# Kernel tuning notes

Measured on AMD Instinct MI355X. Metric: run time of the kernel, lower is better.

## Reference

```python
import jax, jax.numpy as jnp
import numpy as np

STRIDE = 2

def setup_inputs() -> dict:
    key = jax.random.key(0)
    k1, k2 = jax.random.split(key)
    x = jax.random.normal(k1, (32, 128, 112, 112), dtype=jnp.float32)
    # matches nn.init.normal_(std=0.1)
    weight = jax.random.normal(k2, (256, 128, 3, 3), dtype=jnp.float32) * 0.1
    return {"x": x, "weight": weight}

def reference(x, weight):
    # Equivalent to the tile-loop: valid cross-correlation, no bias, stride=STRIDE.
    # x: (B, Cin, H, W); weight: (Cout, Cin, k, k) -> (B, Cout, w, w)
    return jax.lax.conv_general_dilated(
        x, weight,
        window_strides=(STRIDE, STRIDE),
        padding="VALID",
        dimension_numbers=("NCHW", "OIHW", "NCHW"),
    )
```

## Files before the change

### kernel.cpp

```cpp
#include <hip/hip_runtime.h>


#define BATCH 32
#define CIN   128
#define H     112
#define W     112
#define COUT  256
#define OH    55
#define OW    55
#define NPIX  (OH*OW)
#define NTOT  (BATCH*NPIX)

#define BN    192
#define NBLK  ((NTOT + BN - 1) / BN)

typedef __bf16 bf16x8 __attribute__((ext_vector_type(8)));
typedef float  f32x4  __attribute__((ext_vector_type(4)));

__device__ __forceinline__ unsigned short f2bf(float f) {
    unsigned u = __float_as_uint(f);
    u += 0x7FFFu + ((u >> 16) & 1u);
    return (unsigned short)(u >> 16);
}

__device__ __forceinline__ void gld_lds16(const void* g, void* l) {
    __builtin_amdgcn_global_load_lds((__attribute__((address_space(1))) void*)g,
                                     (__attribute__((address_space(3))) void*)l,
                                     16, 0, 0);
}

#define XP 136
#define WBLK ((9*COUT*CIN + 255)/256)
__global__ __launch_bounds__(256) void relayout_k(const float* __restrict__ x,
                                                  const float* __restrict__ w,
                                                  unsigned short* __restrict__ xs,
                                                  unsigned short* __restrict__ wt) {
    if (blockIdx.x >= BATCH * H) {
        int o = (blockIdx.x - BATCH * H) * 256 + threadIdx.x;
        if (o < 9 * COUT * CIN) {
            int cin  = o & (CIN - 1);
            int r    = o >> 7;
            int cout = r & (COUT - 1);
            int tap  = r >> 8;
            wt[o] = f2bf(w[((size_t)cout * CIN + cin) * 9 + tap]);
        }
        return;
    }
    __shared__ __align__(16) unsigned short tile[W * XP];
    const int bh = blockIdx.x;
    const int b  = bh / H;
    const int h  = bh - b * H;
    const float* xr = x + (size_t)b * CIN * (H * W) + (size_t)h * W;
    const int t = threadIdx.x;
#pragma unroll
    for (int i = 0; i < 7; ++i) {
        int e  = t + i * 256;
        int cp = e / 28;
        int w4 = e - cp * 28;
        int c  = cp * 2;
        float4 v0 = *(const float4*)(xr + (size_t)c * (H * W) + w4 * 4);
        float4 v1 = *(const float4*)(xr + (size_t)(c + 1) * (H * W) + w4 * 4);
        int c8 = c >> 3;
        int cl = c & 7;
        float a0[4] = {v0.x, v0.y, v0.z, v0.w};
        float a1[4] = {v1.x, v1.y, v1.z, v1.w};
#pragma unroll
        for (int j = 0; j < 4; ++j) {
            int ww  = w4 * 4 + j;
            int idx = ww * XP + ((c8 + 2 * ww) & 15) * 8 + cl;
            *(ushort2*)(tile + idx) = (ushort2){f2bf(a0[j]), f2bf(a1[j])};
        }
    }
    __syncthreads();
    uint4* dst = (uint4*)(xs + (size_t)bh * (W * CIN));
#pragma unroll
    for (int i = 0; i < 7; ++i) {
        int e  = t + i * 256;
        int ww = e >> 4;
        int c8 = e & 15;
        dst[e] = *(const uint4*)(tile + ww * XP + ((c8 + 2 * ww) & 15) * 8);
    }
}

__global__ __launch_bounds__(512, 2) void conv_mfma_k(const unsigned short* __restrict__ xs,
                                                      const unsigned short* __restrict__ wt,
                                                      float* __restrict__ out) {
    __shared__ __align__(16) unsigned short L[2][(COUT + BN) * 64];

    const int tid  = threadIdx.x;
    const int wave = tid >> 6;
    const int lane = tid & 63;
    const int wm   = wave >> 2;
    const int wn   = wave & 3;
    const int lrow = lane & 15;
    const int kg   = lane >> 4;
    const int n0   = blockIdx.x * BN;

    const int rA  = tid >> 3;
    const int sx8 = ((tid & 7) ^ (rA & 7)) * 8;
    int xbr[3];
#pragma unroll
    for (int c = 0; c < 3; ++c) {
        int nn = n0 + c * 64 + rA;
        if (nn >= NTOT) nn = NTOT - 1;
        int b  = nn / NPIX;
        int rp = nn - b * NPIX;
        int oh = rp / OW;
        int ow = rp - oh * OW;
        xbr[c] = ((b * H + 2 * oh) * W + 2 * ow) * CIN;
    }

    auto stage = [&](int kt, int buf) {
        const int tap  = kt >> 1;
        const int cin0 = (kt & 1) * 64;
        const int r    = (tap >= 6) ? 2 : (tap >= 3) ? 1 : 0;
        const int s    = tap - 3 * r;
        const unsigned short* wsrc = wt + tap * (COUT * CIN) + rA * CIN + cin0 + sx8;
        const unsigned short* xsrc = xs + (r * W + s) * CIN + cin0 + sx8;
        unsigned short* lb = &L[buf][0];
#pragma unroll
        for (int c = 0; c < 4; ++c)
            gld_lds16(wsrc + c * 64 * CIN, lb + c * 4096 + wave * 512);
#pragma unroll
        for (int c = 0; c < 3; ++c)
            gld_lds16(xsrc + xbr[c], lb + 16384 + c * 4096 + wave * 512);
    };

    const int aoff = (wm * 128 + lrow) * 64;
    const int boff = COUT * 64 + (wn * 48 + lrow) * 64;
    const int sxk0 = ((0 * 4 + kg) ^ (lrow & 7)) * 8;
    const int sxk1 = ((1 * 4 + kg) ^ (lrow & 7)) * 8;

    f32x4 acc[8][3];
#pragma unroll
    for (int mi = 0; mi < 8; ++mi)
#pragma unroll
        for (int ni = 0; ni < 3; ++ni)
            acc[mi][ni] = (f32x4){0.f, 0.f, 0.f, 0.f};

    stage(0, 0);
    stage(1, 1);

#pragma unroll 2
    for (int kt = 0; kt < 18; ++kt) {
        const int buf = kt & 1;
        if (kt == 17) asm volatile("s_waitcnt vmcnt(0)" ::: "memory");
        else          asm volatile("s_waitcnt vmcnt(7)" ::: "memory");
        asm volatile("s_barrier" ::: "memory");

        const unsigned short* Lb = &L[buf][0];
        bf16x8 a0[8], b0[3], a1[8], b1[3];
#pragma unroll
        for (int mi = 0; mi < 8; ++mi)
            a0[mi] = *(const bf16x8*)(Lb + aoff + mi * 1024 + sxk0);
#pragma unroll
        for (int ni = 0; ni < 3; ++ni)
            b0[ni] = *(const bf16x8*)(Lb + boff + ni * 1024 + sxk0);
        asm volatile("s_barrier" ::: "memory");
#pragma unroll
        for (int mi = 0; mi < 8; ++mi)
            a1[mi] = *(const bf16x8*)(Lb + aoff + mi * 1024 + sxk1);
#pragma unroll
        for (int ni = 0; ni < 3; ++ni)
            b1[ni] = *(const bf16x8*)(Lb + boff + ni * 1024 + sxk1);
        __builtin_amdgcn_s_setprio(1);
#pragma unroll
        for (int mi = 0; mi < 8; ++mi)
#pragma unroll
            for (int ni = 0; ni < 3; ++ni)
                acc[mi][ni] = __builtin_amdgcn_mfma_f32_16x16x32_bf16(a0[mi], b0[ni], acc[mi][ni], 0, 0, 0);
        __builtin_amdgcn_s_setprio(0);
        asm volatile("s_barrier" ::: "memory");
        if (kt + 2 < 18) stage(kt + 2, buf);
        __builtin_amdgcn_s_setprio(1);
#pragma unroll
        for (int mi = 0; mi < 8; ++mi)
#pragma unroll
            for (int ni = 0; ni < 3; ++ni)
                acc[mi][ni] = __builtin_amdgcn_mfma_f32_16x16x32_bf16(a1[mi], b1[ni], acc[mi][ni], 0, 0, 0);
        __builtin_amdgcn_s_setprio(0);
    }

    long obase[3];
    int  okn[3];
#pragma unroll
    for (int ni = 0; ni < 3; ++ni) {
        int nn = n0 + wn * 48 + ni * 16 + lrow;
        okn[ni] = (nn < NTOT);
        if (!okn[ni]) nn = 0;
        int b   = nn / NPIX;
        int pix = nn - b * NPIX;
        obase[ni] = (long)b * (COUT * NPIX) + pix;
    }
    const int mrow = kg * 4;
#pragma unroll
    for (int mi = 0; mi < 8; ++mi) {
#pragma unroll
        for (int rr = 0; rr < 4; ++rr) {
            int  m  = wm * 128 + mi * 16 + mrow + rr;
            long mo = (long)m * NPIX;
#pragma unroll
            for (int ni = 0; ni < 3; ++ni)
                if (okn[ni]) out[obase[ni] + mo] = acc[mi][ni][rr];
        }
    }
}

__global__ __launch_bounds__(256) void direct_k(const float* __restrict__ x,
                                                const float* __restrict__ w,
                                                float* __restrict__ out) {
    const int pix = blockIdx.x * 256 + threadIdx.x;
    if (pix >= NPIX) return;
    const int b = blockIdx.z, cout0 = blockIdx.y * 8;
    const int oh = pix / OW, ow = pix - oh * OW;
    float acc[8];
#pragma unroll
    for (int i = 0; i < 8; ++i) acc[i] = 0.f;
    const float* xbp = x + ((size_t)b * CIN) * (H * W) + (size_t)(oh * 2) * W + ow * 2;
    const float* wb  = w + (size_t)cout0 * (CIN * 9);
    for (int cin = 0; cin < CIN; ++cin) {
        const float* xp = xbp + (size_t)cin * (H * W);
        float xv[9];
#pragma unroll
        for (int r = 0; r < 3; ++r) {
            xv[r * 3 + 0] = xp[r * W + 0];
            xv[r * 3 + 1] = xp[r * W + 1];
            xv[r * 3 + 2] = xp[r * W + 2];
        }
#pragma unroll
        for (int c = 0; c < 8; ++c) {
            const float* wp = wb + (size_t)c * (CIN * 9) + cin * 9;
#pragma unroll
            for (int k = 0; k < 9; ++k) acc[c] = fmaf(wp[k], xv[k], acc[c]);
        }
    }
    const size_t ob = ((size_t)b * COUT + cout0) * NPIX + pix;
#pragma unroll
    for (int c = 0; c < 8; ++c) out[ob + (size_t)c * NPIX] = acc[c];
}

extern "C" void kernel_launch(void* const* d_in, const int* in_sizes, int n_in,
                              void* d_out, int out_size, void* d_ws, size_t ws_size,
                              hipStream_t stream) {
    const float* x = (const float*)d_in[0];
    const float* w = (const float*)d_in[1];
    float* out = (float*)d_out;

    const size_t xs_elems = (size_t)BATCH * H * W * CIN;
    const size_t wt_elems = (size_t)9 * COUT * CIN;
    const size_t need = (xs_elems + wt_elems) * 2;

    if (ws_size >= need) {
        unsigned short* xs = (unsigned short*)d_ws;
        unsigned short* wt = xs + xs_elems;
        relayout_k<<<dim3(BATCH * H + WBLK), dim3(256), 0, stream>>>(x, w, xs, wt);
        conv_mfma_k<<<dim3(NBLK), dim3(512), 0, stream>>>(xs, wt, out);
    } else {
        dim3 grid((NPIX + 255) / 256, COUT / 8, BATCH);
        direct_k<<<grid, dim3(256), 0, stream>>>(x, w, out);
    }
}
```

Measured before the change: 382.3 us.

## Interleave LDS fragment loads with MFMA halves and swizzle blocks across XCDs

Splits each k-step's A fragments into low and high halves, so MFMA work on one half overlaps the LDS reads for the next half. This also cuts live A registers from 16 vectors to 8. Block indices are remapped so that contiguous pixel tiles land on the same XCD, which should improve L2 reuse of the overlapping input windows. The finer interleave relies on compiler scheduling and could add LDS wait stalls between the MFMA groups.

```diff
diff --git a/kernel.cpp b/kernel.cpp
--- a/kernel.cpp
+++ b/kernel.cpp
@@ -94,7 +94,12 @@
     const int wn   = wave & 3;
     const int lrow = lane & 15;
     const int kg   = lane >> 4;
-    const int n0   = blockIdx.x * BN;
+
+    const int xcd = blockIdx.x & 7;
+    const int lin = blockIdx.x >> 3;
+    const int q = NBLK >> 3, r = NBLK & 7;
+    const int bswz = (xcd < r ? xcd * (q + 1) : r * (q + 1) + (xcd - r) * q) + lin;
+    const int n0 = bswz * BN;
 
     const int rA  = tid >> 3;
     const int sx8 = ((tid & 7) ^ (rA & 7)) * 8;
@@ -113,10 +118,10 @@
     auto stage = [&](int kt, int buf) {
         const int tap  = kt >> 1;
         const int cin0 = (kt & 1) * 64;
-        const int r    = (tap >= 6) ? 2 : (tap >= 3) ? 1 : 0;
-        const int s    = tap - 3 * r;
+        const int r2   = (tap >= 6) ? 2 : (tap >= 3) ? 1 : 0;
+        const int s    = tap - 3 * r2;
         const unsigned short* wsrc = wt + tap * (COUT * CIN) + rA * CIN + cin0 + sx8;
-        const unsigned short* xsrc = xs + (r * W + s) * CIN + cin0 + sx8;
+        const unsigned short* xsrc = xs + (r2 * W + s) * CIN + cin0 + sx8;
         unsigned short* lb = &L[buf][0];
 #pragma unroll
         for (int c = 0; c < 4; ++c)
@@ -149,35 +154,55 @@
         asm volatile("s_barrier" ::: "memory");
 
         const unsigned short* Lb = &L[buf][0];
-        bf16x8 a0[8], b0[3], a1[8], b1[3];
-#pragma unroll
-        for (int mi = 0; mi < 8; ++mi)
-            a0[mi] = *(const bf16x8*)(Lb + aoff + mi * 1024 + sxk0);
+        bf16x8 aL[4], aH[4], b0[3], b1[3];
+#pragma unroll
+        for (int mi = 0; mi < 4; ++mi)
+            aL[mi] = *(const bf16x8*)(Lb + aoff + mi * 1024 + sxk0);
 #pragma unroll
         for (int ni = 0; ni < 3; ++ni)
             b0[ni] = *(const bf16x8*)(Lb + boff + ni * 1024 + sxk0);
         asm volatile("s_barrier" ::: "memory");
-#pragma unroll
-        for (int mi = 0; mi < 8; ++mi)
-            a1[mi] = *(const bf16x8*)(Lb + aoff + mi * 1024 + sxk1);
+        __builtin_amdgcn_s_setprio(1);
+#pragma unroll
+        for (int mi = 0; mi < 4; ++mi)
+#pragma unroll
+            for (int ni = 0; ni < 3; ++ni)
+                acc[mi][ni] = __builtin_amdgcn_mfma_f32_16x16x32_bf16(aL[mi], b0[ni], acc[mi][ni], 0, 0, 0);
+        __builtin_amdgcn_s_setprio(0);
+#pragma unroll
+        for (int mi = 0; mi < 4; ++mi)
+            aH[mi] = *(const bf16x8*)(Lb + aoff + (mi + 4) * 1024 + sxk0);
+        __builtin_amdgcn_s_setprio(1);
+#pragma unroll
+        for (int mi = 0; mi < 4; ++mi)
+#pragma unroll
+            for (int ni = 0; ni < 3; ++ni)
+                acc[mi + 4][ni] = __builtin_amdgcn_mfma_f32_16x16x32_bf16(aH[mi], b0[ni], acc[mi + 4][ni], 0, 0, 0);
+        __builtin_amdgcn_s_setprio(0);
+#pragma unroll
+        for (int mi = 0; mi < 4; ++mi)
+            aL[mi] = *(const bf16x8*)(Lb + aoff + mi * 1024 + sxk1);
 #pragma unroll
         for (int ni = 0; ni < 3; ++ni)
             b1[ni] = *(const bf16x8*)(Lb + boff + ni * 1024 + sxk1);
         __builtin_amdgcn_s_setprio(1);
 #pragma unroll
-        for (int mi = 0; mi < 8; ++mi)
-#pragma unroll
-            for (int ni = 0; ni < 3; ++ni)
-                acc[mi][ni] = __builtin_amdgcn_mfma_f32_16x16x32_bf16(a0[mi], b0[ni], acc[mi][ni], 0, 0, 0);
-        __builtin_amdgcn_s_setprio(0);
+        for (int mi = 0; mi < 4; ++mi)
+#pragma unroll
+            for (int ni = 0; ni < 3; ++ni)
+                acc[mi][ni] = __builtin_amdgcn_mfma_f32_16x16x32_bf16(aL[mi], b1[ni], acc[mi][ni], 0, 0, 0);
+        __builtin_amdgcn_s_setprio(0);
+#pragma unroll
+        for (int mi = 0; mi < 4; ++mi)
+            aH[mi] = *(const bf16x8*)(Lb + aoff + (mi + 4) * 1024 + sxk1);
         asm volatile("s_barrier" ::: "memory");
         if (kt + 2 < 18) stage(kt + 2, buf);
         __builtin_amdgcn_s_setprio(1);
 #pragma unroll
-        for (int mi = 0; mi < 8; ++mi)
-#pragma unroll
-            for (int ni = 0; ni < 3; ++ni)
-                acc[mi][ni] = __builtin_amdgcn_mfma_f32_16x16x32_bf16(a1[mi], b1[ni], acc[mi][ni], 0, 0, 0);
+        for (int mi = 0; mi < 4; ++mi)
+#pragma unroll
+            for (int ni = 0; ni < 3; ++ni)
+                acc[mi + 4][ni] = __builtin_amdgcn_mfma_f32_16x16x32_bf16(aH[mi], b1[ni], acc[mi + 4][ni], 0, 0, 0);
         __builtin_amdgcn_s_setprio(0);
     }
 
@@ -197,7 +222,7 @@
     for (int mi = 0; mi < 8; ++mi) {
 #pragma unroll
         for (int rr = 0; rr < 4; ++rr) {
-            int  m  = wm * 128 + mi * 16 + mrow + rr;
+            int  m  = mi * 16 + mrow + rr + wm * 128;
             long mo = (long)m * NPIX;
 #pragma unroll
             for (int ni = 0; ni < 3; ++ni)
```

Result: no change. 381.8 us (-0.1%).

## Split output-channel tile into two 128-row blocks with XCD-aware block swizzle

Applied to the files above, without the earlier changes.

Each block of the implicit-GEMM conv now covers 128 of the 256 output channels with 4 waves (256 threads) instead of 8 waves, which doubles the grid. A chiplet-aware index remap places the two channel halves of the same pixel tile on the same XCD so they can share the input tile through L2. The inner loop now loads both k-halves from LDS before a single barrier, removing the mid-iteration barrier, and then issues all MFMAs together. The cost is twice as many input-tile loads per output, since each pixel tile is fetched by two blocks, and a larger per-wave MFMA footprint of 4x6.

```diff
diff --git a/kernel.cpp b/kernel.cpp
--- a/kernel.cpp
+++ b/kernel.cpp
@@ -11,8 +11,10 @@
 #define NPIX  (OH*OW)
 #define NTOT  (BATCH*NPIX)
 
+#define BM    128
 #define BN    192
-#define NBLK  ((NTOT + BN - 1) / BN)
+#define NB_N  ((NTOT + BN - 1) / BN)
+#define NBLK  (2 * NB_N)
 
 typedef __bf16 bf16x8 __attribute__((ext_vector_type(8)));
 typedef float  f32x4  __attribute__((ext_vector_type(4)));
@@ -82,26 +84,32 @@
     }
 }
 
-__global__ __launch_bounds__(512, 2) void conv_mfma_k(const unsigned short* __restrict__ xs,
+__global__ __launch_bounds__(256, 2) void conv_mfma_k(const unsigned short* __restrict__ xs,
                                                       const unsigned short* __restrict__ wt,
                                                       float* __restrict__ out) {
-    __shared__ __align__(16) unsigned short L[2][(COUT + BN) * 64];
+    __shared__ __align__(16) unsigned short L[2][(BM + BN) * 64];
 
     const int tid  = threadIdx.x;
     const int wave = tid >> 6;
     const int lane = tid & 63;
-    const int wm   = wave >> 2;
-    const int wn   = wave & 3;
+    const int wm   = wave >> 1;
+    const int wn   = wave & 1;
     const int lrow = lane & 15;
     const int kg   = lane >> 4;
-    const int n0   = blockIdx.x * BN;
+
+    const int xcd = blockIdx.x & 7;
+    const int lin = blockIdx.x >> 3;
+    const int q = NBLK >> 3, r = NBLK & 7;
+    const int bswz = (xcd < r ? xcd * (q + 1) : r * (q + 1) + (xcd - r) * q) + lin;
+    const int m0 = (bswz & 1) * BM;
+    const int n0 = (bswz >> 1) * BN;
 
     const int rA  = tid >> 3;
     const int sx8 = ((tid & 7) ^ (rA & 7)) * 8;
-    int xbr[3];
-#pragma unroll
-    for (int c = 0; c < 3; ++c) {
-        int nn = n0 + c * 64 + rA;
+    int xbr[6];
+#pragma unroll
+    for (int c = 0; c < 6; ++c) {
+        int nn = n0 + c * 32 + rA;
         if (nn >= NTOT) nn = NTOT - 1;
         int b  = nn / NPIX;
         int rp = nn - b * NPIX;
@@ -113,29 +121,29 @@
     auto stage = [&](int kt, int buf) {
         const int tap  = kt >> 1;
         const int cin0 = (kt & 1) * 64;
-        const int r    = (tap >= 6) ? 2 : (tap >= 3) ? 1 : 0;
-        const int s    = tap - 3 * r;
-        const unsigned short* wsrc = wt + tap * (COUT * CIN) + rA * CIN + cin0 + sx8;
-        const unsigned short* xsrc = xs + (r * W + s) * CIN + cin0 + sx8;
+        const int r2   = (tap >= 6) ? 2 : (tap >= 3) ? 1 : 0;
+        const int s    = tap - 3 * r2;
+        const unsigned short* wsrc = wt + tap * (COUT * CIN) + (m0 + rA) * CIN + cin0 + sx8;
+        const unsigned short* xsrc = xs + (r2 * W + s) * CIN + cin0 + sx8;
         unsigned short* lb = &L[buf][0];
 #pragma unroll
         for (int c = 0; c < 4; ++c)
-            gld_lds16(wsrc + c * 64 * CIN, lb + c * 4096 + wave * 512);
-#pragma unroll
-        for (int c = 0; c < 3; ++c)
-            gld_lds16(xsrc + xbr[c], lb + 16384 + c * 4096 + wave * 512);
+            gld_lds16(wsrc + c * 32 * CIN, lb + c * 2048 + wave * 512);
+#pragma unroll
+        for (int c = 0; c < 6; ++c)
+            gld_lds16(xsrc + xbr[c], lb + BM * 64 + c * 2048 + wave * 512);
     };
 
-    const int aoff = (wm * 128 + lrow) * 64;
-    const int boff = COUT * 64 + (wn * 48 + lrow) * 64;
+    const int aoff = (wm * 64 + lrow) * 64;
+    const int boff = BM * 64 + (wn * 96 + lrow) * 64;
     const int sxk0 = ((0 * 4 + kg) ^ (lrow & 7)) * 8;
     const int sxk1 = ((1 * 4 + kg) ^ (lrow & 7)) * 8;
 
-    f32x4 acc[8][3];
-#pragma unroll
-    for (int mi = 0; mi < 8; ++mi)
-#pragma unroll
-        for (int ni = 0; ni < 3; ++ni)
+    f32x4 acc[4][6];
+#pragma unroll
+    for (int mi = 0; mi < 4; ++mi)
+#pragma unroll
+        for (int ni = 0; ni < 6; ++ni)
             acc[mi][ni] = (f32x4){0.f, 0.f, 0.f, 0.f};
 
     stage(0, 0);
@@ -145,47 +153,42 @@
     for (int kt = 0; kt < 18; ++kt) {
         const int buf = kt & 1;
         if (kt == 17) asm volatile("s_waitcnt vmcnt(0)" ::: "memory");
-        else          asm volatile("s_waitcnt vmcnt(7)" ::: "memory");
+        else          asm volatile("s_waitcnt vmcnt(10)" ::: "memory");
         asm volatile("s_barrier" ::: "memory");
 
         const unsigned short* Lb = &L[buf][0];
-        bf16x8 a0[8], b0[3], a1[8], b1[3];
-#pragma unroll
-        for (int mi = 0; mi < 8; ++mi)
+        bf16x8 a0[4], a1[4], b0[6], b1[6];
+#pragma unroll
+        for (int mi = 0; mi < 4; ++mi) {
             a0[mi] = *(const bf16x8*)(Lb + aoff + mi * 1024 + sxk0);
-#pragma unroll
-        for (int ni = 0; ni < 3; ++ni)
+            a1[mi] = *(const bf16x8*)(Lb + aoff + mi * 1024 + sxk1);
+        }
+#pragma unroll
+        for (int ni = 0; ni < 6; ++ni) {
             b0[ni] = *(const bf16x8*)(Lb + boff + ni * 1024 + sxk0);
-        asm volatile("s_barrier" ::: "memory");
-#pragma unroll
-        for (int mi = 0; mi < 8; ++mi)
-            a1[mi] = *(const bf16x8*)(Lb + aoff + mi * 1024 + sxk1);
-#pragma unroll
-        for (int ni = 0; ni < 3; ++ni)
             b1[ni] = *(const bf16x8*)(Lb + boff + ni * 1024 + sxk1);
-        __builtin_amdgcn_s_setprio(1);
-#pragma unroll
-        for (int mi = 0; mi < 8; ++mi)
-#pragma unroll
-            for (int ni = 0; ni < 3; ++ni)
-                acc[mi][ni] = __builtin_amdgcn_mfma_f32_16x16x32_bf16(a0[mi], b0[ni], acc[mi][ni], 0, 0, 0);
-        __builtin_amdgcn_s_setprio(0);
+        }
         asm volatile("s_barrier" ::: "memory");
         if (kt + 2 < 18) stage(kt + 2, buf);
         __builtin_amdgcn_s_setprio(1);
 #pragma unroll
-        for (int mi = 0; mi < 8; ++mi)
-#pragma unroll
-            for (int ni = 0; ni < 3; ++ni)
+        for (int mi = 0; mi < 4; ++mi)
+#pragma unroll
+            for (int ni = 0; ni < 6; ++ni)
+                acc[mi][ni] = __builtin_amdgcn_mfma_f32_16x16x32_bf16(a0[mi], b0[ni], acc[mi][ni], 0, 0, 0);
+#pragma unroll
+        for (int mi = 0; mi < 4; ++mi)
+#pragma unroll
+            for (int ni = 0; ni < 6; ++ni)
                 acc[mi][ni] = __builtin_amdgcn_mfma_f32_16x16x32_bf16(a1[mi], b1[ni], acc[mi][ni], 0, 0, 0);
         __builtin_amdgcn_s_setprio(0);
     }
 
-    long obase[3];
-    int  okn[3];
-#pragma unroll
-    for (int ni = 0; ni < 3; ++ni) {
-        int nn = n0 + wn * 48 + ni * 16 + lrow;
+    long obase[6];
+    int  okn[6];
+#pragma unroll
+    for (int ni = 0; ni < 6; ++ni) {
+        int nn = n0 + wn * 96 + ni * 16 + lrow;
         okn[ni] = (nn < NTOT);
         if (!okn[ni]) nn = 0;
         int b   = nn / NPIX;
@@ -194,13 +197,13 @@
     }
     const int mrow = kg * 4;
 #pragma unroll
-    for (int mi = 0; mi < 8; ++mi) {
+    for (int mi = 0; mi < 4; ++mi) {
 #pragma unroll
         for (int rr = 0; rr < 4; ++rr) {
-            int  m  = wm * 128 + mi * 16 + mrow + rr;
+            int  m  = m0 + wm * 64 + mi * 16 + mrow + rr;
             long mo = (long)m * NPIX;
 #pragma unroll
-            for (int ni = 0; ni < 3; ++ni)
+            for (int ni = 0; ni < 6; ++ni)
                 if (okn[ni]) out[obase[ni] + mo] = acc[mi][ni][rr];
         }
     }
@@ -254,7 +257,7 @@
         unsigned short* xs = (unsigned short*)d_ws;
         unsigned short* wt = xs + xs_elems;
         relayout_k<<<dim3(BATCH * H + WBLK), dim3(256), 0, stream>>>(x, w, xs, wt);
-        conv_mfma_k<<<dim3(NBLK), dim3(512), 0, stream>>>(xs, wt, out);
+        conv_mfma_k<<<dim3(NBLK), dim3(256), 0, stream>>>(xs, wt, out);
     } else {
         dim3 grid((NPIX + 255) / 256, COUT / 8, BATCH);
         direct_k<<<grid, dim3(256), 0, stream>>>(x, w, out);
```

Result: no change. 383.8 us (+0.4%).
